# Optimization experiments

Measured on AMD Instinct MI355X. Metric: run time of the kernel, lower is better.

## Reference

```python
import jax, jax.numpy as jnp
import numpy as np

N = 50000      # nodes
E = 800000     # edges
DIN = 128      # input feature dim
H = 128        # hidden_channels (cfg.gnn.dim_inner)
DOUT = 64      # output classes
EPS = 1e-5


def setup_inputs() -> dict:
    key = jax.random.key(0)
    ks = jax.random.split(key, 24)
    w = lambda k, s: jax.random.normal(k, s, jnp.float32) * 0.05
    return {
        "x": jax.random.normal(ks[0], (N, DIN), jnp.float32),
        "edge_index": jax.random.randint(ks[1], (2, E), 0, N, jnp.int32),
        # pre-processing 2-layer MLP
        "pre_w1": w(ks[2], (DIN, H)), "pre_b1": jnp.zeros((H,), jnp.float32),
        "pre_w2": w(ks[3], (H, H)),   "pre_b2": jnp.zeros((H,), jnp.float32),
        # 3 GCNConv layers
        "conv_w0": w(ks[4], (H, H)), "conv_b0": jnp.zeros((H,), jnp.float32),
        "conv_w1": w(ks[5], (H, H)), "conv_b1": jnp.zeros((H,), jnp.float32),
        "conv_w2": w(ks[6], (H, H)), "conv_b2": jnp.zeros((H,), jnp.float32),
        # BatchNorm affine params (after conv0 and conv1)
        "bn_g0": jnp.ones((H,), jnp.float32), "bn_b0": jnp.zeros((H,), jnp.float32),
        "bn_g1": jnp.ones((H,), jnp.float32), "bn_b1": jnp.zeros((H,), jnp.float32),
        # post-processing 2-layer MLP
        "post_w1": w(ks[7], (H, H)),    "post_b1": jnp.zeros((H,), jnp.float32),
        "post_w2": w(ks[8], (H, DOUT)), "post_b2": jnp.zeros((DOUT,), jnp.float32),
    }


def _gcn_norm(edge_index):
    # add self loops, compute symmetric normalization D^-1/2 A D^-1/2
    loops = jnp.arange(N, dtype=edge_index.dtype)
    src = jnp.concatenate([edge_index[0], loops])  # [E+N]
    dst = jnp.concatenate([edge_index[1], loops])
    deg = jax.ops.segment_sum(jnp.ones_like(src, jnp.float32), dst, num_segments=N)
    dinv = jnp.where(deg > 0, jax.lax.rsqrt(deg), 0.0)
    norm = dinv[src] * dinv[dst]                   # [E+N]
    return src, dst, norm


def _gcn_conv(x, W, b, src, dst, norm):
    h = x @ W                                      # [N, F_out]
    msg = h[src] * norm[:, None]                   # gather + scale  [E+N, F_out]
    return jax.ops.segment_sum(msg, dst, num_segments=N) + b


def _bn(x, g, b):
    m = x.mean(axis=0)
    v = x.var(axis=0)  # biased, as torch BN uses for normalization
    return (x - m) * jax.lax.rsqrt(v + EPS) * g + b


def reference(x, edge_index, pre_w1, pre_b1, pre_w2, pre_b2,
              conv_w0, conv_b0, conv_w1, conv_b1, conv_w2, conv_b2,
              bn_g0, bn_b0, bn_g1, bn_b1,
              post_w1, post_b1, post_w2, post_b2):
    src, dst, norm = _gcn_norm(edge_index)
    # pre-proc MLP (dropout=0)
    h = jax.nn.relu(x @ pre_w1 + pre_b1)
    h = jax.nn.relu(h @ pre_w2 + pre_b2)
    # conv -> BN -> relu (x2), then final conv
    h = jax.nn.relu(_bn(_gcn_conv(h, conv_w0, conv_b0, src, dst, norm), bn_g0, bn_b0))
    h = jax.nn.relu(_bn(_gcn_conv(h, conv_w1, conv_b1, src, dst, norm), bn_g1, bn_b1))
    h = _gcn_conv(h, conv_w2, conv_b2, src, dst, norm)
    # post-proc MLP
    h = jax.nn.relu(h @ post_w1 + post_b1)
    return h @ post_w2 + post_b2  # [N, DOUT] node logits
```

## Files before the change

kernel.cpp:

```cpp
#include <hip/hip_runtime.h>
#include <hip/hip_bf16.h>

#define NN 50000
#define EE 800000
#define DIN 128
#define HH 128
#define DOUT 64
#define BN_EPS 1e-5f

typedef __attribute__((ext_vector_type(8))) short short8;
typedef __attribute__((ext_vector_type(4))) float floatx4;

static inline size_t align_up(size_t x, size_t a) { return (x + a - 1) & ~(a - 1); }

__device__ __forceinline__ float bf2f(ushort u) {
    uint v = ((uint)u) << 16;
    return __builtin_bit_cast(float, v);
}
__device__ __forceinline__ float bf2f_lo(uint u) { return __builtin_bit_cast(float, u << 16); }
__device__ __forceinline__ float bf2f_hi(uint u) { return __builtin_bit_cast(float, u & 0xffff0000u); }
__device__ __forceinline__ ushort f2bf(float f) {
    uint u = __builtin_bit_cast(uint, f);
    u += 0x7fff + ((u >> 16) & 1);
    return (ushort)(u >> 16);
}
__device__ __forceinline__ uint pack_bf2(float lo, float hi) {
    return (uint)f2bf(lo) | ((uint)f2bf(hi) << 16);
}

__global__ void tcast_all_kernel(const float* __restrict__ s0, const float* __restrict__ s1,
                                 const float* __restrict__ s2, const float* __restrict__ s3,
                                 const float* __restrict__ s4, const float* __restrict__ s5,
                                 const float* __restrict__ s6,
                                 ushort* __restrict__ d0, ushort* __restrict__ d1,
                                 ushort* __restrict__ d2, ushort* __restrict__ d3,
                                 ushort* __restrict__ d4, ushort* __restrict__ d5,
                                 ushort* __restrict__ d6) {
    const float* src; ushort* dst; int F = 128;
    switch (blockIdx.y) {
        case 0: src = s0; dst = d0; break;
        case 1: src = s1; dst = d1; break;
        case 2: src = s2; dst = d2; break;
        case 3: src = s3; dst = d3; break;
        case 4: src = s4; dst = d4; break;
        case 5: src = s5; dst = d5; break;
        default: src = s6; dst = d6; F = 64; break;
    }
    int t = blockIdx.x * 256 + threadIdx.x;
    if (t >= F * 128) return;
    int f = t >> 7, k = t & 127;
    dst[t] = f2bf(src[(size_t)k * F + f]);
}

__global__ void cnt_kernel(const int* __restrict__ ei, int* __restrict__ cnt,
                           int* __restrict__ rank, int E) {
    int e = (blockIdx.x * 256 + threadIdx.x) * 4;
    if (e + 3 < E) {
        int4 d = *(const int4*)(ei + E + e);
        int4 r;
        r.x = atomicAdd(&cnt[d.x], 1);
        r.y = atomicAdd(&cnt[d.y], 1);
        r.z = atomicAdd(&cnt[d.z], 1);
        r.w = atomicAdd(&cnt[d.w], 1);
        *(int4*)(rank + e) = r;
    } else {
        for (; e < E; ++e) rank[e] = atomicAdd(&cnt[ei[E + e]], 1);
    }
}

__device__ __forceinline__ void block_scan256(int v, int* lsum, int& excl, int& total) {
    int lane = threadIdx.x & 63, w = threadIdx.x >> 6;
    int inc = v;
    #pragma unroll
    for (int s = 1; s < 64; s <<= 1) {
        int t = __shfl_up(inc, s);
        if (lane >= s) inc += t;
    }
    if (lane == 63) lsum[w] = inc;
    __syncthreads();
    int pre = 0;
    #pragma unroll
    for (int k = 0; k < 4; ++k)
        if (k < w) pre += lsum[k];
    excl = pre + inc - v;
    total = lsum[0] + lsum[1] + lsum[2] + lsum[3];
    __syncthreads();
}

__global__ void scan_part_kernel(const int* __restrict__ cnt, int* __restrict__ off,
                                 int* __restrict__ bsum, float* __restrict__ dinv, int n) {
    __shared__ int lsum[4];
    int i = blockIdx.x * 256 + threadIdx.x;
    int v = (i < n) ? cnt[i] : 0;
    int excl, total;
    block_scan256(v, lsum, excl, total);
    if (i < n) {
        off[i] = excl;
        dinv[i] = rsqrtf((float)(v + 1));
    }
    if (threadIdx.x == 0) bsum[blockIdx.x] = total;
}

__global__ void scan_bsum_kernel(int* __restrict__ bsum, int nb) {
    __shared__ int lsum[4];
    int t = threadIdx.x;
    int v = (t < nb) ? bsum[t] : 0;
    int excl, total;
    block_scan256(v, lsum, excl, total);
    if (t < nb) bsum[t] = excl;
}

__global__ void scan_add_kernel(int* __restrict__ off, const int* __restrict__ bsum, int n) {
    int i = blockIdx.x * 256 + threadIdx.x;
    if (i < n) off[i] += bsum[blockIdx.x];
    if (i == 0) off[n] = EE;
}

__global__ void fill_kernel(const int* __restrict__ ei, const int* __restrict__ off,
                            const int* __restrict__ rank, int2* __restrict__ csr,
                            const float* __restrict__ dinv, int E) {
    int e = (blockIdx.x * 256 + threadIdx.x) * 2;
    if (e + 1 < E) {
        int2 s2 = *(const int2*)(ei + e);
        int2 d2 = *(const int2*)(ei + E + e);
        int2 r2 = *(const int2*)(rank + e);
        float wa = dinv[s2.x] * dinv[d2.x];
        float wb = dinv[s2.y] * dinv[d2.y];
        int pa = off[d2.x] + r2.x;
        int pb = off[d2.y] + r2.y;
        csr[pa] = make_int2(s2.x, __builtin_bit_cast(int, wa));
        csr[pb] = make_int2(s2.y, __builtin_bit_cast(int, wb));
    } else if (e < E) {
        int s = ei[e];
        int d = ei[E + e];
        float w = dinv[s] * dinv[d];
        csr[off[d] + rank[e]] = make_int2(s, __builtin_bit_cast(int, w));
    }
}

template <int NCG>
__device__ __forceinline__ void zero_acc(floatx4 (&acc)[2][NCG]) {
    #pragma unroll
    for (int rg = 0; rg < 2; ++rg)
        #pragma unroll
        for (int cg = 0; cg < NCG; ++cg)
            acc[rg][cg] = (floatx4){0.f, 0.f, 0.f, 0.f};
}

template <int FO>
__device__ __forceinline__ void stage_w(const ushort* __restrict__ Wt, uint4* Wl, int tid) {
    #pragma unroll
    for (int c = tid; c < FO * 16; c += 256) {
        int f = c >> 4, kb = c & 15;
        Wl[f * 16 + (kb ^ (f & 15))] = ((const uint4*)Wt)[c];
    }
}

template <int NCG>
__device__ __forceinline__ void gemm_step(const uint4* Xl, const uint4* Wl,
                                          floatx4 (&acc)[2][NCG], int wv, int lr, int lk) {
    #pragma unroll
    for (int ks = 0; ks < 4; ++ks) {
        int kb = ks * 4 + lk;
        int swz = kb ^ lr;
        short8 a0 = *(const short8*)&Xl[(wv * 32 + lr) * 16 + swz];
        short8 a1 = *(const short8*)&Xl[(wv * 32 + 16 + lr) * 16 + swz];
        #pragma unroll
        for (int cg = 0; cg < NCG; ++cg) {
            short8 b = *(const short8*)&Wl[(cg * 16 + lr) * 16 + swz];
            acc[0][cg] = __builtin_amdgcn_mfma_f32_16x16x32_bf16(a0, b, acc[0][cg], 0, 0, 0);
            acc[1][cg] = __builtin_amdgcn_mfma_f32_16x16x32_bf16(a1, b, acc[1][cg], 0, 0, 0);
        }
    }
}

template <int NCG>
__device__ __forceinline__ void write_h(floatx4 (&acc)[2][NCG], uint4* Xl,
                                        const float* __restrict__ bias,
                                        int wv, int lr, int lk) {
    ushort* Xs = (ushort*)Xl;
    #pragma unroll
    for (int rg = 0; rg < 2; ++rg)
        #pragma unroll
        for (int cg = 0; cg < NCG; ++cg) {
            int col = cg * 16 + lr;
            float bv = bias[col];
            #pragma unroll
            for (int j = 0; j < 4; ++j) {
                int row = wv * 32 + rg * 16 + lk * 4 + j;
                float o = fmaxf(acc[rg][cg][j] + bv, 0.f);
                Xs[(row * 16 + ((col >> 3) ^ (row & 15))) * 8 + (col & 7)] = f2bf(o);
            }
        }
}

template <int FOUT, bool RELU, bool BIAS, bool OUTF32>
__device__ __forceinline__ void epilogue(floatx4 (&acc)[2][FOUT / 16],
                                         const float* __restrict__ bias, void* Yout,
                                         int row0, int n, int wv, int lr, int lk) {
    #pragma unroll
    for (int rg = 0; rg < 2; ++rg) {
        int rbase = row0 + wv * 32 + rg * 16 + lk * 4;
        #pragma unroll
        for (int cg = 0; cg < FOUT / 16; ++cg) {
            int col = cg * 16 + lr;
            float bv = BIAS ? bias[col] : 0.f;
            #pragma unroll
            for (int j = 0; j < 4; ++j) {
                int r = rbase + j;
                if (r < n) {
                    float o = acc[rg][cg][j] + bv;
                    if (RELU) o = fmaxf(o, 0.f);
                    if (OUTF32)
                        ((float*)Yout)[(size_t)r * FOUT + col] = o;
                    else
                        ((ushort*)Yout)[(size_t)r * FOUT + col] = f2bf(o);
                }
            }
        }
    }
}

__global__ __launch_bounds__(256, 2) void fused_pre_kernel(
    const float* __restrict__ Xg, const ushort* __restrict__ W1t, const float* __restrict__ b1,
    const ushort* __restrict__ W2t, const float* __restrict__ b2,
    const ushort* __restrict__ W3t, ushort* __restrict__ Yout, int n) {
    __shared__ uint4 lds4[4096];
    uint4* Xl = lds4;
    uint4* Wl = lds4 + 2048;
    const int tid = threadIdx.x;
    const int row0 = blockIdx.x * 128;

    for (int c = tid; c < 2048; c += 256) {
        int r = c >> 4, kb = c & 15;
        int row = row0 + r;
        uint4 v = make_uint4(0, 0, 0, 0);
        if (row < n) {
            const float4* p = (const float4*)(Xg + (size_t)row * 128 + kb * 8);
            float4 x0 = p[0], x1 = p[1];
            v.x = pack_bf2(x0.x, x0.y);
            v.y = pack_bf2(x0.z, x0.w);
            v.z = pack_bf2(x1.x, x1.y);
            v.w = pack_bf2(x1.z, x1.w);
        }
        Xl[r * 16 + (kb ^ (r & 15))] = v;
    }
    stage_w<128>(W1t, Wl, tid);
    __syncthreads();

    const int wv = tid >> 6, lane = tid & 63;
    const int lr = lane & 15, lk = lane >> 4;

    floatx4 acc[2][8];
    zero_acc<8>(acc);
    gemm_step<8>(Xl, Wl, acc, wv, lr, lk);
    __syncthreads();
    write_h<8>(acc, Xl, b1, wv, lr, lk);
    stage_w<128>(W2t, Wl, tid);
    __syncthreads();

    zero_acc<8>(acc);
    gemm_step<8>(Xl, Wl, acc, wv, lr, lk);
    __syncthreads();
    write_h<8>(acc, Xl, b2, wv, lr, lk);
    stage_w<128>(W3t, Wl, tid);
    __syncthreads();

    zero_acc<8>(acc);
    gemm_step<8>(Xl, Wl, acc, wv, lr, lk);
    epilogue<128, false, false, false>(acc, nullptr, Yout, row0, n, wv, lr, lk);
}

__global__ __launch_bounds__(256, 2) void fused_post_kernel(
    const ushort* __restrict__ Xg, const ushort* __restrict__ W1t, const float* __restrict__ b1,
    const ushort* __restrict__ W2t, const float* __restrict__ b2,
    float* __restrict__ Yout, int n) {
    __shared__ uint4 lds4[4096];
    uint4* Xl = lds4;
    uint4* Wl = lds4 + 2048;
    const int tid = threadIdx.x;
    const int row0 = blockIdx.x * 128;

    for (int c = tid; c < 2048; c += 256) {
        int r = c >> 4, kb = c & 15;
        int row = row0 + r;
        uint4 v = make_uint4(0, 0, 0, 0);
        if (row < n) v = ((const uint4*)(Xg + (size_t)row * 128))[kb];
        Xl[r * 16 + (kb ^ (r & 15))] = v;
    }
    stage_w<128>(W1t, Wl, tid);
    __syncthreads();

    const int wv = tid >> 6, lane = tid & 63;
    const int lr = lane & 15, lk = lane >> 4;

    floatx4 acc[2][8];
    zero_acc<8>(acc);
    gemm_step<8>(Xl, Wl, acc, wv, lr, lk);
    __syncthreads();
    write_h<8>(acc, Xl, b1, wv, lr, lk);
    stage_w<64>(W2t, Wl, tid);
    __syncthreads();

    floatx4 acc2[2][4];
    zero_acc<4>(acc2);
    gemm_step<4>(Xl, Wl, acc2, wv, lr, lk);
    epilogue<64, false, true, true>(acc2, b2, Yout, row0, n, wv, lr, lk);
}

__global__ __launch_bounds__(256, 2) void gemm_bnf_kernel(
    const ushort* __restrict__ Xg, const ushort* __restrict__ Wt,
    const float* __restrict__ sums, const float* __restrict__ sumsq,
    const float* __restrict__ g, const float* __restrict__ bb,
    ushort* __restrict__ Yout, int n) {
    __shared__ uint4 lds4[4096];
    __shared__ float scf[128], shf[128];
    uint4* Xl = lds4;
    uint4* Wl = lds4 + 2048;
    const int tid = threadIdx.x;
    const int row0 = blockIdx.x * 128;

    if (tid < 128) {
        const float inv_n = 1.0f / (float)NN;
        float m = sums[tid] * inv_n;
        float var = sumsq[tid] * inv_n - m * m;
        float sc = g[tid] * rsqrtf(var + BN_EPS);
        scf[tid] = sc;
        shf[tid] = bb[tid] - m * sc;
    }
    stage_w<128>(Wt, Wl, tid);
    __syncthreads();

    for (int c = tid; c < 2048; c += 256) {
        int r = c >> 4, kb = c & 15;
        int row = row0 + r;
        uint4 v = make_uint4(0, 0, 0, 0);
        if (row < n) v = ((const uint4*)(Xg + (size_t)row * 128))[kb];
        uint a[4] = {v.x, v.y, v.z, v.w};
        #pragma unroll
        for (int p = 0; p < 4; ++p) {
            int f0 = kb * 8 + p * 2;
            float lo = fmaxf(fmaf(bf2f_lo(a[p]), scf[f0], shf[f0]), 0.f);
            float hi = fmaxf(fmaf(bf2f_hi(a[p]), scf[f0 + 1], shf[f0 + 1]), 0.f);
            a[p] = pack_bf2(lo, hi);
        }
        Xl[r * 16 + (kb ^ (r & 15))] = make_uint4(a[0], a[1], a[2], a[3]);
    }
    __syncthreads();

    const int wv = tid >> 6, lane = tid & 63;
    const int lr = lane & 15, lk = lane >> 4;

    floatx4 acc[2][8];
    zero_acc<8>(acc);
    gemm_step<8>(Xl, Wl, acc, wv, lr, lk);
    epilogue<128, false, false, false>(acc, nullptr, Yout, row0, n, wv, lr, lk);
}

__global__ __launch_bounds__(256) void agg16_kernel(const ushort* __restrict__ h,
                                                    const float* __restrict__ dinv,
                                                    const int* __restrict__ off,
                                                    const int2* __restrict__ csr,
                                                    const float* __restrict__ bias,
                                                    ushort* __restrict__ out, int n) {
    int i = (blockIdx.x * 256 + threadIdx.x) >> 6;
    if (i >= n) return;
    int lane = threadIdx.x & 63;

    const uint* __restrict__ hq = (const uint*)h;
    float di = dinv[i];
    float sw = di * di;
    uint u = hq[(size_t)i * 64 + lane];
    float a0 = bf2f_lo(u) * sw, a1 = bf2f_hi(u) * sw;

    const int s0 = off[i], s1 = off[i + 1];
    int j = s0;
    for (; j + 8 <= s1; j += 8) {
        int2 e0 = csr[j + 0], e1 = csr[j + 1], e2 = csr[j + 2], e3 = csr[j + 3];
        int2 e4 = csr[j + 4], e5 = csr[j + 5], e6 = csr[j + 6], e7 = csr[j + 7];
        uint u0 = hq[(size_t)e0.x * 64 + lane];
        uint u1 = hq[(size_t)e1.x * 64 + lane];
        uint u2 = hq[(size_t)e2.x * 64 + lane];
        uint u3 = hq[(size_t)e3.x * 64 + lane];
        uint u4 = hq[(size_t)e4.x * 64 + lane];
        uint u5 = hq[(size_t)e5.x * 64 + lane];
        uint u6 = hq[(size_t)e6.x * 64 + lane];
        uint u7 = hq[(size_t)e7.x * 64 + lane];
        float w0 = __builtin_bit_cast(float, e0.y), w1 = __builtin_bit_cast(float, e1.y);
        float w2 = __builtin_bit_cast(float, e2.y), w3 = __builtin_bit_cast(float, e3.y);
        float w4 = __builtin_bit_cast(float, e4.y), w5 = __builtin_bit_cast(float, e5.y);
        float w6 = __builtin_bit_cast(float, e6.y), w7 = __builtin_bit_cast(float, e7.y);
        a0 += bf2f_lo(u0) * w0 + bf2f_lo(u1) * w1 + bf2f_lo(u2) * w2 + bf2f_lo(u3) * w3
            + bf2f_lo(u4) * w4 + bf2f_lo(u5) * w5 + bf2f_lo(u6) * w6 + bf2f_lo(u7) * w7;
        a1 += bf2f_hi(u0) * w0 + bf2f_hi(u1) * w1 + bf2f_hi(u2) * w2 + bf2f_hi(u3) * w3
            + bf2f_hi(u4) * w4 + bf2f_hi(u5) * w5 + bf2f_hi(u6) * w6 + bf2f_hi(u7) * w7;
    }
    for (; j + 4 <= s1; j += 4) {
        int2 e0 = csr[j + 0], e1 = csr[j + 1], e2 = csr[j + 2], e3 = csr[j + 3];
        uint u0 = hq[(size_t)e0.x * 64 + lane];
        uint u1 = hq[(size_t)e1.x * 64 + lane];
        uint u2 = hq[(size_t)e2.x * 64 + lane];
        uint u3 = hq[(size_t)e3.x * 64 + lane];
        float w0 = __builtin_bit_cast(float, e0.y), w1 = __builtin_bit_cast(float, e1.y);
        float w2 = __builtin_bit_cast(float, e2.y), w3 = __builtin_bit_cast(float, e3.y);
        a0 += bf2f_lo(u0) * w0 + bf2f_lo(u1) * w1 + bf2f_lo(u2) * w2 + bf2f_lo(u3) * w3;
        a1 += bf2f_hi(u0) * w0 + bf2f_hi(u1) * w1 + bf2f_hi(u2) * w2 + bf2f_hi(u3) * w3;
    }
    for (; j < s1; ++j) {
        int2 e = csr[j];
        float w = __builtin_bit_cast(float, e.y);
        uint uv = hq[(size_t)e.x * 64 + lane];
        a0 += bf2f_lo(uv) * w;
        a1 += bf2f_hi(uv) * w;
    }

    float2 b2 = ((const float2*)bias)[lane];
    a0 += b2.x; a1 += b2.y;
    __builtin_nontemporal_store(pack_bf2(a0, a1), (uint*)out + (size_t)i * 64 + lane);
}

__global__ __launch_bounds__(256) void bn_stats16_kernel(const ushort* __restrict__ x,
                                                         float* __restrict__ sums,
                                                         float* __restrict__ sumsq, int n) {
    __shared__ float ls[128], lq[128];
    int tid = threadIdx.x;
    if (tid < 128) { ls[tid] = 0.f; lq[tid] = 0.f; }
    __syncthreads();
    int fg = tid & 15, rg = tid >> 4;
    float s[8] = {}, q[8] = {};
    for (int r = blockIdx.x * 16 + rg; r < n; r += gridDim.x * 16) {
        uint4 v = ((const uint4*)(x + (size_t)r * 128))[fg];
        uint a[4] = {v.x, v.y, v.z, v.w};
        #pragma unroll
        for (int p = 0; p < 4; ++p) {
            float lo = bf2f_lo(a[p]), hi = bf2f_hi(a[p]);
            s[2 * p] += lo;     q[2 * p] += lo * lo;
            s[2 * p + 1] += hi; q[2 * p + 1] += hi * hi;
        }
    }
    #pragma unroll
    for (int k = 0; k < 8; ++k) {
        atomicAdd(&ls[fg * 8 + k], s[k]);
        atomicAdd(&lq[fg * 8 + k], q[k]);
    }
    __syncthreads();
    if (tid < 128) {
        atomicAdd(&sums[tid], ls[tid]);
        atomicAdd(&sumsq[tid], lq[tid]);
    }
}

extern "C" void kernel_launch(void* const* d_in, const int* in_sizes, int n_in,
                              void* d_out, int out_size, void* d_ws, size_t ws_size,
                              hipStream_t stream) {
    const float* x        = (const float*)d_in[0];
    const int*   ei       = (const int*)d_in[1];
    const float* pre_w1   = (const float*)d_in[2];
    const float* pre_b1   = (const float*)d_in[3];
    const float* pre_w2   = (const float*)d_in[4];
    const float* pre_b2   = (const float*)d_in[5];
    const float* conv_w0  = (const float*)d_in[6];
    const float* conv_b0  = (const float*)d_in[7];
    const float* conv_w1  = (const float*)d_in[8];
    const float* conv_b1  = (const float*)d_in[9];
    const float* conv_w2  = (const float*)d_in[10];
    const float* conv_b2  = (const float*)d_in[11];
    const float* bn_g0    = (const float*)d_in[12];
    const float* bn_b0    = (const float*)d_in[13];
    const float* bn_g1    = (const float*)d_in[14];
    const float* bn_b1    = (const float*)d_in[15];
    const float* post_w1  = (const float*)d_in[16];
    const float* post_b1  = (const float*)d_in[17];
    const float* post_w2  = (const float*)d_in[18];
    const float* post_b2  = (const float*)d_in[19];
    float* out = (float*)d_out;

    const int n = NN, E = EE;
    const int NB = (n + 255) / 256;

    char* w = (char*)d_ws;
    int* cnt    = (int*)w;   w += (size_t)n * 4;
    float* bns0 = (float*)w;
    float* bnq0 = bns0 + 128;
    float* bns1 = bns0 + 256;
    float* bnq1 = bns0 + 384;
    w += align_up(512 * 4, 512);
    int* rank   = (int*)w;   w += align_up((size_t)E * 4, 512);
    int* bsum   = (int*)w;   w += align_up(256 * 4, 512);
    int* off    = (int*)w;   w += align_up((size_t)(n + 1) * 4, 512);
    float* dinv = (float*)w; w += align_up((size_t)n * 4, 512);
    int2* csr   = (int2*)w;  w += align_up((size_t)E * 8, 512);
    ushort* wt_pre1  = (ushort*)w; w += align_up(128 * 128 * 2, 512);
    ushort* wt_pre2  = (ushort*)w; w += align_up(128 * 128 * 2, 512);
    ushort* wt_c0    = (ushort*)w; w += align_up(128 * 128 * 2, 512);
    ushort* wt_c1    = (ushort*)w; w += align_up(128 * 128 * 2, 512);
    ushort* wt_c2    = (ushort*)w; w += align_up(128 * 128 * 2, 512);
    ushort* wt_post1 = (ushort*)w; w += align_up(128 * 128 * 2, 512);
    ushort* wt_post2 = (ushort*)w; w += align_up(64 * 128 * 2, 512);
    ushort* P = (ushort*)w; w += align_up((size_t)n * 128 * 2, 512);
    ushort* Q = (ushort*)w; w += align_up((size_t)n * 128 * 2, 512);
    ushort* R = (ushort*)w; w += align_up((size_t)n * 128 * 2, 512);

    hipMemsetAsync(cnt, 0, (size_t)n * 4 + 512 * 4, stream);

    tcast_all_kernel<<<dim3(64, 7), 256, 0, stream>>>(
        pre_w1, pre_w2, conv_w0, conv_w1, conv_w2, post_w1, post_w2,
        wt_pre1, wt_pre2, wt_c0, wt_c1, wt_c2, wt_post1, wt_post2);

    cnt_kernel<<<(E / 4 + 255) / 256, 256, 0, stream>>>(ei, cnt, rank, E);
    scan_part_kernel<<<NB, 256, 0, stream>>>(cnt, off, bsum, dinv, n);
    scan_bsum_kernel<<<1, 256, 0, stream>>>(bsum, NB);
    scan_add_kernel<<<NB, 256, 0, stream>>>(off, bsum, n);
    fill_kernel<<<(E / 2 + 255) / 256, 256, 0, stream>>>(ei, off, rank, csr, dinv, E);

    const int gb = (n + 127) / 128;
    const int agg_blocks = (n * 64 + 255) / 256;

    fused_pre_kernel<<<gb, 256, 0, stream>>>(x, wt_pre1, pre_b1, wt_pre2, pre_b2, wt_c0, P, n);
    agg16_kernel<<<agg_blocks, 256, 0, stream>>>(P, dinv, off, csr, conv_b0, Q, n);
    bn_stats16_kernel<<<256, 256, 0, stream>>>(Q, bns0, bnq0, n);

    gemm_bnf_kernel<<<gb, 256, 0, stream>>>(Q, wt_c1, bns0, bnq0, bn_g0, bn_b0, P, n);
    agg16_kernel<<<agg_blocks, 256, 0, stream>>>(P, dinv, off, csr, conv_b1, R, n);
    bn_stats16_kernel<<<256, 256, 0, stream>>>(R, bns1, bnq1, n);

    gemm_bnf_kernel<<<gb, 256, 0, stream>>>(R, wt_c2, bns1, bnq1, bn_g1, bn_b1, P, n);
    agg16_kernel<<<agg_blocks, 256, 0, stream>>>(P, dinv, off, csr, conv_b2, Q, n);

    fused_post_kernel<<<gb, 256, 0, stream>>>(Q, wt_post1, post_b1, wt_post2, post_b2, out, n);
}
```

Baseline: 380.3 us.

## Halve GEMM row tile to 64 rows and use nontemporal CSR loads/stores

The fused MLP/GEMM kernels now process 64 rows per block instead of 128: one 16-row MFMA group per wave, less LDS (48KB instead of 64KB) and fewer accumulator registers, with launch bounds raised to 3 blocks per CU. This gives more blocks and higher occupancy, but the weights are restaged per block twice as often. Separately, CSR edges are written and read as packed 64-bit nontemporal accesses, and the cnt kernel's rank writes become nontemporal scalar stores. The aim is to reduce cache pollution in the aggregation, at some risk of losing L2 reuse of the CSR between the three aggregation passes.

Measured after the change: 417.4 us. +9.8%, slower.

```diff
diff --git a/kernel.cpp b/kernel.cpp
--- a/kernel.cpp
+++ b/kernel.cpp
@@ -10,6 +10,7 @@
 
 typedef __attribute__((ext_vector_type(8))) short short8;
 typedef __attribute__((ext_vector_type(4))) float floatx4;
+typedef unsigned long long u64;
 
 static inline size_t align_up(size_t x, size_t a) { return (x + a - 1) & ~(a - 1); }
 
@@ -62,7 +63,10 @@
         r.y = atomicAdd(&cnt[d.y], 1);
         r.z = atomicAdd(&cnt[d.z], 1);
         r.w = atomicAdd(&cnt[d.w], 1);
-        *(int4*)(rank + e) = r;
+        __builtin_nontemporal_store(r.x, rank + e + 0);
+        __builtin_nontemporal_store(r.y, rank + e + 1);
+        __builtin_nontemporal_store(r.z, rank + e + 2);
+        __builtin_nontemporal_store(r.w, rank + e + 3);
     } else {
         for (; e < E; ++e) rank[e] = atomicAdd(&cnt[ei[E + e]], 1);
     }
@@ -128,8 +132,10 @@
         float wb = dinv[s2.y] * dinv[d2.y];
         int pa = off[d2.x] + r2.x;
         int pb = off[d2.y] + r2.y;
-        csr[pa] = make_int2(s2.x, __builtin_bit_cast(int, wa));
-        csr[pb] = make_int2(s2.y, __builtin_bit_cast(int, wb));
+        u64 va = (u64)(uint)s2.x | ((u64)(uint)__builtin_bit_cast(uint, wa) << 32);
+        u64 vb = (u64)(uint)s2.y | ((u64)(uint)__builtin_bit_cast(uint, wb) << 32);
+        __builtin_nontemporal_store(va, (u64*)(csr + pa));
+        __builtin_nontemporal_store(vb, (u64*)(csr + pb));
     } else if (e < E) {
         int s = ei[e];
         int d = ei[E + e];
@@ -139,12 +145,10 @@
 }
 
 template <int NCG>
-__device__ __forceinline__ void zero_acc(floatx4 (&acc)[2][NCG]) {
-    #pragma unroll
-    for (int rg = 0; rg < 2; ++rg)
-        #pragma unroll
-        for (int cg = 0; cg < NCG; ++cg)
-            acc[rg][cg] = (floatx4){0.f, 0.f, 0.f, 0.f};
+__device__ __forceinline__ void zero_acc(floatx4 (&acc)[NCG]) {
+    #pragma unroll
+    for (int cg = 0; cg < NCG; ++cg)
+        acc[cg] = (floatx4){0.f, 0.f, 0.f, 0.f};
 }
 
 template <int FO>
@@ -158,80 +162,73 @@
 
 template <int NCG>
 __device__ __forceinline__ void gemm_step(const uint4* Xl, const uint4* Wl,
-                                          floatx4 (&acc)[2][NCG], int wv, int lr, int lk) {
+                                          floatx4 (&acc)[NCG], int wv, int lr, int lk) {
     #pragma unroll
     for (int ks = 0; ks < 4; ++ks) {
         int kb = ks * 4 + lk;
         int swz = kb ^ lr;
-        short8 a0 = *(const short8*)&Xl[(wv * 32 + lr) * 16 + swz];
-        short8 a1 = *(const short8*)&Xl[(wv * 32 + 16 + lr) * 16 + swz];
+        short8 a0 = *(const short8*)&Xl[(wv * 16 + lr) * 16 + swz];
         #pragma unroll
         for (int cg = 0; cg < NCG; ++cg) {
             short8 b = *(const short8*)&Wl[(cg * 16 + lr) * 16 + swz];
-            acc[0][cg] = __builtin_amdgcn_mfma_f32_16x16x32_bf16(a0, b, acc[0][cg], 0, 0, 0);
-            acc[1][cg] = __builtin_amdgcn_mfma_f32_16x16x32_bf16(a1, b, acc[1][cg], 0, 0, 0);
+            acc[cg] = __builtin_amdgcn_mfma_f32_16x16x32_bf16(a0, b, acc[cg], 0, 0, 0);
         }
     }
 }
 
 template <int NCG>
-__device__ __forceinline__ void write_h(floatx4 (&acc)[2][NCG], uint4* Xl,
+__device__ __forceinline__ void write_h(floatx4 (&acc)[NCG], uint4* Xl,
                                         const float* __restrict__ bias,
                                         int wv, int lr, int lk) {
     ushort* Xs = (ushort*)Xl;
     #pragma unroll
-    for (int rg = 0; rg < 2; ++rg)
+    for (int cg = 0; cg < NCG; ++cg) {
+        int col = cg * 16 + lr;
+        float bv = bias[col];
         #pragma unroll
-        for (int cg = 0; cg < NCG; ++cg) {
-            int col = cg * 16 + lr;
-            float bv = bias[col];
-            #pragma unroll
-            for (int j = 0; j < 4; ++j) {
-                int row = wv * 32 + rg * 16 + lk * 4 + j;
-                float o = fmaxf(acc[rg][cg][j] + bv, 0.f);
-                Xs[(row * 16 + ((col >> 3) ^ (row & 15))) * 8 + (col & 7)] = f2bf(o);
+        for (int j = 0; j < 4; ++j) {
+            int row = wv * 16 + lk * 4 + j;
+            float o = fmaxf(acc[cg][j] + bv, 0.f);
+            Xs[(row * 16 + ((col >> 3) ^ (row & 15))) * 8 + (col & 7)] = f2bf(o);
+        }
+    }
+}
+
+template <int FOUT, bool RELU, bool BIAS, bool OUTF32>
+__device__ __forceinline__ void epilogue(floatx4 (&acc)[FOUT / 16],
+                                         const float* __restrict__ bias, void* Yout,
+                                         int row0, int n, int wv, int lr, int lk) {
+    int rbase = row0 + wv * 16 + lk * 4;
+    #pragma unroll
+    for (int cg = 0; cg < FOUT / 16; ++cg) {
+        int col = cg * 16 + lr;
+        float bv = BIAS ? bias[col] : 0.f;
+        #pragma unroll
+        for (int j = 0; j < 4; ++j) {
+            int r = rbase + j;
+            if (r < n) {
+                float o = acc[cg][j] + bv;
+                if (RELU) o = fmaxf(o, 0.f);
+                if (OUTF32)
+                    ((float*)Yout)[(size_t)r * FOUT + col] = o;
+                else
+                    ((ushort*)Yout)[(size_t)r * FOUT + col] = f2bf(o);
             }
         }
-}
-
-template <int FOUT, bool RELU, bool BIAS, bool OUTF32>
-__device__ __forceinline__ void epilogue(floatx4 (&acc)[2][FOUT / 16],
-                                         const float* __restrict__ bias, void* Yout,
-                                         int row0, int n, int wv, int lr, int lk) {
-    #pragma unroll
-    for (int rg = 0; rg < 2; ++rg) {
-        int rbase = row0 + wv * 32 + rg * 16 + lk * 4;
-        #pragma unroll
-        for (int cg = 0; cg < FOUT / 16; ++cg) {
-            int col = cg * 16 + lr;
-            float bv = BIAS ? bias[col] : 0.f;
-            #pragma unroll
-            for (int j = 0; j < 4; ++j) {
-                int r = rbase + j;
-                if (r < n) {
-                    float o = acc[rg][cg][j] + bv;
-                    if (RELU) o = fmaxf(o, 0.f);
-                    if (OUTF32)
-                        ((float*)Yout)[(size_t)r * FOUT + col] = o;
-                    else
-                        ((ushort*)Yout)[(size_t)r * FOUT + col] = f2bf(o);
-                }
-            }
-        }
-    }
-}
-
-__global__ __launch_bounds__(256, 2) void fused_pre_kernel(
+    }
+}
+
+__global__ __launch_bounds__(256, 3) void fused_pre_kernel(
     const float* __restrict__ Xg, const ushort* __restrict__ W1t, const float* __restrict__ b1,
     const ushort* __restrict__ W2t, const float* __restrict__ b2,
     const ushort* __restrict__ W3t, ushort* __restrict__ Yout, int n) {
-    __shared__ uint4 lds4[4096];
+    __shared__ uint4 lds4[3072];
     uint4* Xl = lds4;
-    uint4* Wl = lds4 + 2048;
+    uint4* Wl = lds4 + 1024;
     const int tid = threadIdx.x;
-    const int row0 = blockIdx.x * 128;
-
-    for (int c = tid; c < 2048; c += 256) {
+    const int row0 = blockIdx.x * 64;
+
+    for (int c = tid; c < 1024; c += 256) {
         int r = c >> 4, kb = c & 15;
         int row = row0 + r;
         uint4 v = make_uint4(0, 0, 0, 0);
@@ -251,7 +248,7 @@
     const int wv = tid >> 6, lane = tid & 63;
     const int lr = lane & 15, lk = lane >> 4;
 
-    floatx4 acc[2][8];
+    floatx4 acc[8];
     zero_acc<8>(acc);
     gemm_step<8>(Xl, Wl, acc, wv, lr, lk);
     __syncthreads();
@@ -271,17 +268,17 @@
     epilogue<128, false, false, false>(acc, nullptr, Yout, row0, n, wv, lr, lk);
 }
 
-__global__ __launch_bounds__(256, 2) void fused_post_kernel(
+__global__ __launch_bounds__(256, 3) void fused_post_kernel(
     const ushort* __restrict__ Xg, const ushort* __restrict__ W1t, const float* __restrict__ b1,
     const ushort* __restrict__ W2t, const float* __restrict__ b2,
     float* __restrict__ Yout, int n) {
-    __shared__ uint4 lds4[4096];
+    __shared__ uint4 lds4[3072];
     uint4* Xl = lds4;
-    uint4* Wl = lds4 + 2048;
+    uint4* Wl = lds4 + 1024;
     const int tid = threadIdx.x;
-    const int row0 = blockIdx.x * 128;
-
-    for (int c = tid; c < 2048; c += 256) {
+    const int row0 = blockIdx.x * 64;
+
+    for (int c = tid; c < 1024; c += 256) {
         int r = c >> 4, kb = c & 15;
         int row = row0 + r;
         uint4 v = make_uint4(0, 0, 0, 0);
@@ -294,7 +291,7 @@
     const int wv = tid >> 6, lane = tid & 63;
     const int lr = lane & 15, lk = lane >> 4;
 
-    floatx4 acc[2][8];
+    floatx4 acc[8];
     zero_acc<8>(acc);
     gemm_step<8>(Xl, Wl, acc, wv, lr, lk);
     __syncthreads();
@@ -302,23 +299,23 @@
     stage_w<64>(W2t, Wl, tid);
     __syncthreads();
 
-    floatx4 acc2[2][4];
+    floatx4 acc2[4];
     zero_acc<4>(acc2);
     gemm_step<4>(Xl, Wl, acc2, wv, lr, lk);
     epilogue<64, false, true, true>(acc2, b2, Yout, row0, n, wv, lr, lk);
 }
 
-__global__ __launch_bounds__(256, 2) void gemm_bnf_kernel(
+__global__ __launch_bounds__(256, 3) void gemm_bnf_kernel(
     const ushort* __restrict__ Xg, const ushort* __restrict__ Wt,
     const float* __restrict__ sums, const float* __restrict__ sumsq,
     const float* __restrict__ g, const float* __restrict__ bb,
     ushort* __restrict__ Yout, int n) {
-    __shared__ uint4 lds4[4096];
+    __shared__ uint4 lds4[3072];
     __shared__ float scf[128], shf[128];
     uint4* Xl = lds4;
-    uint4* Wl = lds4 + 2048;
+    uint4* Wl = lds4 + 1024;
     const int tid = threadIdx.x;
-    const int row0 = blockIdx.x * 128;
+    const int row0 = blockIdx.x * 64;
 
     if (tid < 128) {
         const float inv_n = 1.0f / (float)NN;
@@ -331,7 +328,7 @@
     stage_w<128>(Wt, Wl, tid);
     __syncthreads();
 
-    for (int c = tid; c < 2048; c += 256) {
+    for (int c = tid; c < 1024; c += 256) {
         int r = c >> 4, kb = c & 15;
         int row = row0 + r;
         uint4 v = make_uint4(0, 0, 0, 0);
@@ -351,7 +348,7 @@
     const int wv = tid >> 6, lane = tid & 63;
     const int lr = lane & 15, lk = lane >> 4;
 
-    floatx4 acc[2][8];
+    floatx4 acc[8];
     zero_acc<8>(acc);
     gemm_step<8>(Xl, Wl, acc, wv, lr, lk);
     epilogue<128, false, false, false>(acc, nullptr, Yout, row0, n, wv, lr, lk);
@@ -368,6 +365,7 @@
     int lane = threadIdx.x & 63;
 
     const uint* __restrict__ hq = (const uint*)h;
+    const u64* __restrict__ ce = (const u64*)csr;
     float di = dinv[i];
     float sw = di * di;
     uint u = hq[(size_t)i * 64 + lane];
@@ -376,40 +374,55 @@
     const int s0 = off[i], s1 = off[i + 1];
     int j = s0;
     for (; j + 8 <= s1; j += 8) {
-        int2 e0 = csr[j + 0], e1 = csr[j + 1], e2 = csr[j + 2], e3 = csr[j + 3];
-        int2 e4 = csr[j + 4], e5 = csr[j + 5], e6 = csr[j + 6], e7 = csr[j + 7];
-        uint u0 = hq[(size_t)e0.x * 64 + lane];
-        uint u1 = hq[(size_t)e1.x * 64 + lane];
-        uint u2 = hq[(size_t)e2.x * 64 + lane];
-        uint u3 = hq[(size_t)e3.x * 64 + lane];
-        uint u4 = hq[(size_t)e4.x * 64 + lane];
-        uint u5 = hq[(size_t)e5.x * 64 + lane];
-        uint u6 = hq[(size_t)e6.x * 64 + lane];
-        uint u7 = hq[(size_t)e7.x * 64 + lane];
-        float w0 = __builtin_bit_cast(float, e0.y), w1 = __builtin_bit_cast(float, e1.y);
-        float w2 = __builtin_bit_cast(float, e2.y), w3 = __builtin_bit_cast(float, e3.y);
-        float w4 = __builtin_bit_cast(float, e4.y), w5 = __builtin_bit_cast(float, e5.y);
-        float w6 = __builtin_bit_cast(float, e6.y), w7 = __builtin_bit_cast(float, e7.y);
+        u64 e0 = __builtin_nontemporal_load(ce + j + 0);
+        u64 e1 = __builtin_nontemporal_load(ce + j + 1);
+        u64 e2 = __builtin_nontemporal_load(ce + j + 2);
+        u64 e3 = __builtin_nontemporal_load(ce + j + 3);
+        u64 e4 = __builtin_nontemporal_load(ce + j + 4);
+        u64 e5 = __builtin_nontemporal_load(ce + j + 5);
+        u64 e6 = __builtin_nontemporal_load(ce + j + 6);
+        u64 e7 = __builtin_nontemporal_load(ce + j + 7);
+        uint u0 = hq[(size_t)(uint)e0 * 64 + lane];
+        uint u1 = hq[(size_t)(uint)e1 * 64 + lane];
+        uint u2 = hq[(size_t)(uint)e2 * 64 + lane];
+        uint u3 = hq[(size_t)(uint)e3 * 64 + lane];
+        uint u4 = hq[(size_t)(uint)e4 * 64 + lane];
+        uint u5 = hq[(size_t)(uint)e5 * 64 + lane];
+        uint u6 = hq[(size_t)(uint)e6 * 64 + lane];
+        uint u7 = hq[(size_t)(uint)e7 * 64 + lane];
+        float w0 = __builtin_bit_cast(float, (uint)(e0 >> 32));
+        float w1 = __builtin_bit_cast(float, (uint)(e1 >> 32));
+        float w2 = __builtin_bit_cast(float, (uint)(e2 >> 32));
+        float w3 = __builtin_bit_cast(float, (uint)(e3 >> 32));
+        float w4 = __builtin_bit_cast(float, (uint)(e4 >> 32));
+        float w5 = __builtin_bit_cast(float, (uint)(e5 >> 32));
+        float w6 = __builtin_bit_cast(float, (uint)(e6 >> 32));
+        float w7 = __builtin_bit_cast(float, (uint)(e7 >> 32));
         a0 += bf2f_lo(u0) * w0 + bf2f_lo(u1) * w1 + bf2f_lo(u2) * w2 + bf2f_lo(u3) * w3
             + bf2f_lo(u4) * w4 + bf2f_lo(u5) * w5 + bf2f_lo(u6) * w6 + bf2f_lo(u7) * w7;
         a1 += bf2f_hi(u0) * w0 + bf2f_hi(u1) * w1 + bf2f_hi(u2) * w2 + bf2f_hi(u3) * w3
             + bf2f_hi(u4) * w4 + bf2f_hi(u5) * w5 + bf2f_hi(u6) * w6 + bf2f_hi(u7) * w7;
     }
     for (; j + 4 <= s1; j += 4) {
-        int2 e0 = csr[j + 0], e1 = csr[j + 1], e2 = csr[j + 2], e3 = csr[j + 3];
-        uint u0 = hq[(size_t)e0.x * 64 + lane];
-        uint u1 = hq[(size_t)e1.x * 64 + lane];
-        uint u2 = hq[(size_t)e2.x * 64 + lane];
-        uint u3 = hq[(size_t)e3.x * 64 + lane];
-        float w0 = __builtin_bit_cast(float, e0.y), w1 = __builtin_bit_cast(float, e1.y);
-        float w2 = __builtin_bit_cast(float, e2.y), w3 = __builtin_bit_cast(float, e3.y);
+        u64 e0 = __builtin_nontemporal_load(ce + j + 0);
+        u64 e1 = __builtin_nontemporal_load(ce + j + 1);
+        u64 e2 = __builtin_nontemporal_load(ce + j + 2);
+        u64 e3 = __builtin_nontemporal_load(ce + j + 3);
+        uint u0 = hq[(size_t)(uint)e0 * 64 + lane];
+        uint u1 = hq[(size_t)(uint)e1 * 64 + lane];
+        uint u2 = hq[(size_t)(uint)e2 * 64 + lane];
+        uint u3 = hq[(size_t)(uint)e3 * 64 + lane];
+        float w0 = __builtin_bit_cast(float, (uint)(e0 >> 32));
+        float w1 = __builtin_bit_cast(float, (uint)(e1 >> 32));
+        float w2 = __builtin_bit_cast(float, (uint)(e2 >> 32));
+        float w3 = __builtin_bit_cast(float, (uint)(e3 >> 32));
         a0 += bf2f_lo(u0) * w0 + bf2f_lo(u1) * w1 + bf2f_lo(u2) * w2 + bf2f_lo(u3) * w3;
         a1 += bf2f_hi(u0) * w0 + bf2f_hi(u1) * w1 + bf2f_hi(u2) * w2 + bf2f_hi(u3) * w3;
     }
     for (; j < s1; ++j) {
-        int2 e = csr[j];
-        float w = __builtin_bit_cast(float, e.y);
-        uint uv = hq[(size_t)e.x * 64 + lane];
+        u64 e = __builtin_nontemporal_load(ce + j);
+        float w = __builtin_bit_cast(float, (uint)(e >> 32));
+        uint uv = hq[(size_t)(uint)e * 64 + lane];
         a0 += bf2f_lo(uv) * w;
         a1 += bf2f_hi(uv) * w;
     }
@@ -513,7 +526,7 @@
     scan_add_kernel<<<NB, 256, 0, stream>>>(off, bsum, n);
     fill_kernel<<<(E / 2 + 255) / 256, 256, 0, stream>>>(ei, off, rank, csr, dinv, E);
 
-    const int gb = (n + 127) / 128;
+    const int gb = (n + 63) / 64;
     const int agg_blocks = (n * 64 + 255) / 256;
 
     fused_pre_kernel<<<gb, 256, 0, stream>>>(x, wt_pre1, pre_b1, wt_pre2, pre_b2, wt_c0, P, n);
```
